# Performance work log

Measured on AMD Instinct MI355X. Metric: run time of the kernel, lower is better.

## Reference

```python
import jax, jax.numpy as jnp
import numpy as np
import math

N_HEAD = 12


def setup_inputs() -> dict:
    key = jax.random.key(0)
    ks = jax.random.split(key, 4)
    B, T, C = 8, 1024, 768
    s = 0.02
    return {
        "x": jax.random.normal(ks[0], (B, T, C), dtype=jnp.float32),
        "attn_mask": jnp.ones((B, T), dtype=jnp.int32),
        "W_attn": jax.random.normal(ks[1], (C, 3 * C), dtype=jnp.float32) * s,
        "b_attn": jnp.zeros((3 * C,), dtype=jnp.float32),
        "W_proj": jax.random.normal(ks[2], (C, C), dtype=jnp.float32) * s,
        "b_proj": jnp.zeros((C,), dtype=jnp.float32),
    }


def reference(x, attn_mask, W_attn, b_attn, W_proj, b_proj):
    B, T, C = x.shape
    hd = C // N_HEAD
    qkv = x @ W_attn + b_attn                      # [B, T, 3C]
    q, k, v = jnp.split(qkv, 3, axis=2)
    # [B, H, T, hd]
    q = q.reshape(B, T, N_HEAD, hd).transpose(0, 2, 1, 3)
    k = k.reshape(B, T, N_HEAD, hd).transpose(0, 2, 1, 3)
    v = v.reshape(B, T, N_HEAD, hd).transpose(0, 2, 1, 3)
    scores = jnp.einsum("bhqd,bhkd->bhqk", q, k) * (1.0 / math.sqrt(hd))
    mask = attn_mask[:, None, None, :]             # [B, 1, 1, T] broadcast over H, q
    scores = jnp.where(mask == 0, -jnp.inf, scores)
    attn = jax.nn.softmax(scores, axis=-1)
    out = jnp.einsum("bhqk,bhkd->bhqd", attn, v)   # [B, H, T, hd]
    out = out.transpose(0, 2, 1, 3).reshape(B, T, C)
    return out @ W_proj + b_proj
```

## Files before the change

kernel.cpp:

```cpp
#include <hip/hip_runtime.h>
#include <math.h>

constexpr int Bsz  = 8;
constexpr int Tseq = 1024;
constexpr int Cdim = 768;
constexpr int NH   = 12;
constexpr int HD   = 64;
constexpr int Mrows = Bsz * Tseq;
constexpr int C3    = 3 * Cdim;

using short8  = __attribute__((ext_vector_type(8))) short;
using s4v     = __attribute__((ext_vector_type(4))) short;
using floatx4 = __attribute__((ext_vector_type(4))) float;

__device__ __forceinline__ unsigned short f32_to_bf16_rn(float f) {
    unsigned int u = __float_as_uint(f);
    unsigned int r = u + 0x7FFFu + ((u >> 16) & 1u);
    return (unsigned short)(r >> 16);
}
__device__ __forceinline__ short8 lds_ld8(const unsigned short* p) {
    s4v a = *(const s4v*)p;
    s4v b = *(const s4v*)(p + 4);
    return __builtin_shufflevector(a, b, 0, 1, 2, 3, 4, 5, 6, 7);
}
__device__ __forceinline__ void lds_st8(unsigned short* p, short8 v) {
    *(s4v*)p       = __builtin_shufflevector(v, v, 0, 1, 2, 3);
    *(s4v*)(p + 4) = __builtin_shufflevector(v, v, 4, 5, 6, 7);
}

#define GLOAD_LDS16(g, l) __builtin_amdgcn_global_load_lds(                    \
    (const __attribute__((address_space(1))) void*)(g),                        \
    (__attribute__((address_space(3))) void*)(l), 16, 0, 0)

__global__ __launch_bounds__(256)
void to_bf16(const float* __restrict__ in, unsigned short* __restrict__ out, int n4)
{
    int t = blockIdx.x * blockDim.x + threadIdx.x;
    if (t >= n4) return;
    float4 v = ((const float4*)in)[t];
    ushort4 o;
    o.x = f32_to_bf16_rn(v.x);
    o.y = f32_to_bf16_rn(v.y);
    o.z = f32_to_bf16_rn(v.z);
    o.w = f32_to_bf16_rn(v.w);
    ((ushort4*)out)[t] = o;
}

__global__ __launch_bounds__(256)
void transpose_bf16(const float* __restrict__ in, unsigned short* __restrict__ out,
                    int K, int N)
{
    __shared__ float tile[32][33];
    const int k0 = blockIdx.y * 32, n0 = blockIdx.x * 32;
    const int tx = threadIdx.x & 31, ty = threadIdx.x >> 5;
    #pragma unroll
    for (int r = ty; r < 32; r += 8)
        tile[r][tx] = in[(size_t)(k0 + r) * N + n0 + tx];
    __syncthreads();
    #pragma unroll
    for (int r = ty; r < 32; r += 8)
        out[(size_t)(n0 + r) * K + k0 + tx] = f32_to_bf16_rn(tile[tx][r]);
}

__global__ __launch_bounds__(256)
void gemm_qkv(const unsigned short* __restrict__ A_g,
              const unsigned short* __restrict__ B_g,
              const float* __restrict__ bias,
              unsigned short* __restrict__ Cb,
              int M, int N, int K)
{
    __shared__ __align__(16) unsigned short Ah[128 * 32];
    __shared__ __align__(16) unsigned short Bh[128 * 32];

    const int tid  = threadIdx.x;
    const int wave = tid >> 6;
    const int lane = tid & 63;
    const int lm   = lane & 15;
    const int quad = lane >> 4;
    const int wy   = wave >> 1, wx = wave & 1;
    const int row0 = blockIdx.y * 128;
    const int col0 = blockIdx.x * 128;

    const int sr  = lane >> 2;
    const int skp = (lane & 3) * 8;

    floatx4 acc[4][4] = {};

    for (int k0 = 0; k0 < K; k0 += 32) {
        __syncthreads();
        #pragma unroll
        for (int s = 0; s < 2; ++s) {
            const int r = (wave * 2 + s) * 16 + sr;
            GLOAD_LDS16(A_g + (size_t)(row0 + r) * K + k0 + skp, &Ah[r * 32 + skp]);
            GLOAD_LDS16(B_g + (size_t)(col0 + r) * K + k0 + skp, &Bh[r * 32 + skp]);
        }
        __syncthreads();

        short8 af[4];
        #pragma unroll
        for (int i = 0; i < 4; ++i)
            af[i] = *(const short8*)&Ah[(wy * 64 + i * 16 + lm) * 32 + quad * 8];
        #pragma unroll
        for (int j = 0; j < 4; ++j) {
            short8 bf = *(const short8*)&Bh[(wx * 64 + j * 16 + lm) * 32 + quad * 8];
            #pragma unroll
            for (int i = 0; i < 4; ++i)
                acc[i][j] = __builtin_amdgcn_mfma_f32_16x16x32_bf16(af[i], bf, acc[i][j], 0, 0, 0);
        }
    }

    __syncthreads();
    unsigned short* wbuf = &Ah[wave * 1024];
    #pragma unroll
    for (int i = 0; i < 4; ++i) {
        #pragma unroll
        for (int j = 0; j < 4; ++j) {
            const float bv = bias[col0 + wx * 64 + j * 16 + lm];
            #pragma unroll
            for (int r = 0; r < 4; ++r)
                wbuf[(quad * 4 + r) * 64 + j * 16 + lm] = f32_to_bf16_rn(acc[i][j][r] + bv);
        }
        #pragma unroll
        for (int p = 0; p < 2; ++p) {
            const int lrow  = p * 8 + (lane >> 3);
            const int lcol8 = (lane & 7) * 8;
            short8 v = lds_ld8(&wbuf[lrow * 64 + lcol8]);
            lds_st8((unsigned short*)&v, v);
            *(short8*)(Cb + (size_t)(row0 + wy * 64 + i * 16 + lrow) * N +
                       col0 + wx * 64 + lcol8) = v;
        }
    }
}

__global__ __launch_bounds__(256)
void gemm_proj(const unsigned short* __restrict__ AO_g,
               const unsigned short* __restrict__ B_g,
               const float* __restrict__ bias,
               float* __restrict__ C,
               int M, int N, int K)
{
    __shared__ __align__(16) unsigned short Ah[128 * 32];
    __shared__ __align__(16) unsigned short Bh[128 * 32];

    const int tid  = threadIdx.x;
    const int wave = tid >> 6;
    const int lane = tid & 63;
    const int lm   = lane & 15;
    const int quad = lane >> 4;
    const int wy   = wave >> 1, wx = wave & 1;
    const int row0 = blockIdx.y * 128;
    const int col0 = blockIdx.x * 128;

    const int sr  = lane >> 2;
    const int skp = (lane & 3) * 8;

    floatx4 acc[4][4] = {};

    for (int k0 = 0; k0 < K; k0 += 32) {
        __syncthreads();
        const int kk   = k0 + skp;
        const int head = kk >> 6;
        const int off  = kk & 63;
        #pragma unroll
        for (int s = 0; s < 2; ++s) {
            const int r = (wave * 2 + s) * 16 + sr;
            GLOAD_LDS16(AO_g + (size_t)head * (Mrows * HD) + (size_t)(row0 + r) * HD + off,
                        &Ah[r * 32 + skp]);
            GLOAD_LDS16(B_g + (size_t)(col0 + r) * K + k0 + skp, &Bh[r * 32 + skp]);
        }
        __syncthreads();

        short8 af[4];
        #pragma unroll
        for (int i = 0; i < 4; ++i)
            af[i] = *(const short8*)&Ah[(wy * 64 + i * 16 + lm) * 32 + quad * 8];
        #pragma unroll
        for (int j = 0; j < 4; ++j) {
            short8 bf = *(const short8*)&Bh[(wx * 64 + j * 16 + lm) * 32 + quad * 8];
            #pragma unroll
            for (int i = 0; i < 4; ++i)
                acc[i][j] = __builtin_amdgcn_mfma_f32_16x16x32_bf16(af[i], bf, acc[i][j], 0, 0, 0);
        }
    }

    #pragma unroll
    for (int j = 0; j < 4; ++j) {
        const int col = col0 + wx * 64 + j * 16 + lm;
        const float bv = bias[col];
        #pragma unroll
        for (int i = 0; i < 4; ++i) {
            const int rowb = row0 + wy * 64 + i * 16 + quad * 4;
            #pragma unroll
            for (int r = 0; r < 4; ++r)
                C[(size_t)(rowb + r) * N + col] = acc[i][j][r] + bv;
        }
    }
}

__global__ __launch_bounds__(256, 2)
void attn_bf16(const unsigned short* __restrict__ qkv,
               const int* __restrict__ mask,
               unsigned short* __restrict__ outh)
{
    constexpr int LDW = 68;
    __shared__ __align__(16) unsigned short Kh[64 * LDW];
    __shared__ __align__(16) unsigned short Vh[64 * LDW];
    __shared__ __align__(16) unsigned short Ph[128 * LDW];
    __shared__ float maskadd[64];

    const int tid  = threadIdx.x;
    const int wave = tid >> 6;
    const int lane = tid & 63;
    const int lm   = lane & 15;
    const int quad = lane >> 4;
    const int idx  = blockIdx.x;
    const int bh   = idx % (Bsz * NH);
    const int qb   = idx / (Bsz * NH);
    const int b    = bh / NH;
    const int h    = bh % NH;
    const int q0   = qb * 128;
    const float scale = 0.125f;

    short8 qf[2][2];
    #pragma unroll
    for (int mt = 0; mt < 2; ++mt) {
        const size_t qrow = (size_t)(b * Tseq + q0 + wave * 32 + mt * 16 + lm) * C3 + h * HD;
        #pragma unroll
        for (int kf = 0; kf < 2; ++kf)
            qf[mt][kf] = *(const short8*)(qkv + qrow + kf * 32 + quad * 8);
    }

    const int sr0 = (tid & 31) * 2;
    const int sc  = (tid >> 5) * 8;

    short8 kh0, kh1, vh0, vh1;
    float  mreg = 0.f;

    {
        const size_t g0 = (size_t)(b * Tseq + sr0) * C3 + Cdim + h * HD + sc;
        kh0 = *(const short8*)(qkv + g0);
        kh1 = *(const short8*)(qkv + g0 + C3);
        vh0 = *(const short8*)(qkv + g0 + Cdim);
        vh1 = *(const short8*)(qkv + g0 + Cdim + C3);
        if (tid < 64) mreg = (mask[b * Tseq + tid] == 0) ? -1e30f : 0.0f;
        lds_st8(&Kh[sr0 * LDW + sc], kh0);
        lds_st8(&Kh[(sr0 + 1) * LDW + sc], kh1);
        #pragma unroll
        for (int i = 0; i < 8; ++i) {
            unsigned int pv = (unsigned int)(unsigned short)vh0[i] |
                              ((unsigned int)(unsigned short)vh1[i] << 16);
            *(unsigned int*)&Vh[(sc + i) * LDW + sr0] = pv;
        }
        if (tid < 64) maskadd[tid] = mreg;
    }
    __syncthreads();

    floatx4 O[2][4] = {};
    float lsum[2] = {0.f, 0.f};
    float madd[4][4];

    for (int kt = 0; kt < Tseq / 64; ++kt) {
        floatx4 S[2][4] = {};
        #pragma unroll
        for (int kf = 0; kf < 2; ++kf) {
            short8 kh[4];
            #pragma unroll
            for (int nt = 0; nt < 4; ++nt)
                kh[nt] = lds_ld8(&Kh[(nt * 16 + lm) * LDW + kf * 32 + quad * 8]);
            #pragma unroll
            for (int mt = 0; mt < 2; ++mt)
                #pragma unroll
                for (int nt = 0; nt < 4; ++nt)
                    S[mt][nt] = __builtin_amdgcn_mfma_f32_16x16x32_bf16(kh[nt], qf[mt][kf], S[mt][nt], 0, 0, 0);
        }
        #pragma unroll
        for (int nt = 0; nt < 4; ++nt)
            #pragma unroll
            for (int r = 0; r < 4; ++r)
                madd[nt][r] = maskadd[nt * 16 + quad * 4 + r];

        if (kt + 1 < Tseq / 64) {
            const size_t g0 = (size_t)(b * Tseq + (kt + 1) * 64 + sr0) * C3 + Cdim + h * HD + sc;
            kh0 = *(const short8*)(qkv + g0);
            kh1 = *(const short8*)(qkv + g0 + C3);
            vh0 = *(const short8*)(qkv + g0 + Cdim);
            vh1 = *(const short8*)(qkv + g0 + Cdim + C3);
            if (tid < 64) mreg = (mask[b * Tseq + (kt + 1) * 64 + tid] == 0) ? -1e30f : 0.0f;
        }

        #pragma unroll
        for (int mt = 0; mt < 2; ++mt) {
            const int prow = (wave * 32 + mt * 16 + lm) * LDW;
            #pragma unroll
            for (int nt = 0; nt < 4; ++nt) {
                ushort4 pk;
                unsigned short* pp = &pk.x;
                #pragma unroll
                for (int r = 0; r < 4; ++r) {
                    float p = __expf(S[mt][nt][r] * scale + madd[nt][r]);
                    lsum[mt] += p;
                    pp[r] = f32_to_bf16_rn(p);
                }
                *(ushort4*)&Ph[prow + nt * 16 + quad * 4] = pk;
            }
        }

        #pragma unroll
        for (int kf = 0; kf < 2; ++kf) {
            short8 pf[2];
            #pragma unroll
            for (int mt = 0; mt < 2; ++mt)
                pf[mt] = lds_ld8(&Ph[(wave * 32 + mt * 16 + lm) * LDW + kf * 32 + quad * 8]);
            #pragma unroll
            for (int dt = 0; dt < 4; ++dt) {
                short8 vh = lds_ld8(&Vh[(dt * 16 + lm) * LDW + kf * 32 + quad * 8]);
                #pragma unroll
                for (int mt = 0; mt < 2; ++mt)
                    O[mt][dt] = __builtin_amdgcn_mfma_f32_16x16x32_bf16(vh, pf[mt], O[mt][dt], 0, 0, 0);
            }
        }

        __syncthreads();
        if (kt + 1 < Tseq / 64) {
            lds_st8(&Kh[sr0 * LDW + sc], kh0);
            lds_st8(&Kh[(sr0 + 1) * LDW + sc], kh1);
            #pragma unroll
            for (int i = 0; i < 8; ++i) {
                unsigned int pv = (unsigned int)(unsigned short)vh0[i] |
                                  ((unsigned int)(unsigned short)vh1[i] << 16);
                *(unsigned int*)&Vh[(sc + i) * LDW + sr0] = pv;
            }
            if (tid < 64) maskadd[tid] = mreg;
        }
        __syncthreads();
    }

    #pragma unroll
    for (int mt = 0; mt < 2; ++mt) {
        lsum[mt] += __shfl_xor(lsum[mt], 16);
        lsum[mt] += __shfl_xor(lsum[mt], 32);
        const float inv_l = 1.0f / lsum[mt];
        const size_t row = (size_t)h * (Mrows * HD) +
                           (size_t)(b * Tseq + q0 + wave * 32 + mt * 16 + lm) * HD;
        #pragma unroll
        for (int dt = 0; dt < 4; ++dt) {
            ushort4 hv;
            unsigned short* hp = &hv.x;
            #pragma unroll
            for (int r = 0; r < 4; ++r)
                hp[r] = f32_to_bf16_rn(O[mt][dt][r] * inv_l);
            *(ushort4*)(outh + row + dt * 16 + quad * 4) = hv;
        }
    }
}

extern "C" void kernel_launch(void* const* d_in, const int* in_sizes, int n_in,
                              void* d_out, int out_size, void* d_ws, size_t ws_size,
                              hipStream_t stream)
{
    const float* x      = (const float*)d_in[0];
    const int*   mask   = (const int*)  d_in[1];
    const float* W_attn = (const float*)d_in[2];
    const float* b_attn = (const float*)d_in[3];
    const float* W_proj = (const float*)d_in[4];
    const float* b_proj = (const float*)d_in[5];
    float* out = (float*)d_out;

    unsigned short* xh    = (unsigned short*)d_ws;
    unsigned short* wat_h = xh    + (size_t)Mrows * Cdim;
    unsigned short* wpt_h = wat_h + (size_t)C3 * Cdim;
    unsigned short* qkvh  = wpt_h + (size_t)Cdim * Cdim;
    unsigned short* aoh   = xh;

    dim3 blk(256);

    to_bf16<<<dim3(Mrows * Cdim / 4 / 256), blk, 0, stream>>>(x, xh, Mrows * Cdim / 4);
    transpose_bf16<<<dim3(C3 / 32, Cdim / 32), blk, 0, stream>>>(W_attn, wat_h, Cdim, C3);
    transpose_bf16<<<dim3(Cdim / 32, Cdim / 32), blk, 0, stream>>>(W_proj, wpt_h, Cdim, Cdim);

    gemm_qkv<<<dim3(C3 / 128, Mrows / 128), blk, 0, stream>>>(
        xh, wat_h, b_attn, qkvh, Mrows, C3, Cdim);

    attn_bf16<<<dim3((Tseq / 128) * Bsz * NH), blk, 0, stream>>>(qkvh, mask, aoh);

    gemm_proj<<<dim3(Cdim / 128, Mrows / 128), blk, 0, stream>>>(
        aoh, wpt_h, b_proj, out, Mrows, Cdim, Cdim);
}
```

Baseline: 227.0 us.

## Double-buffer K/V tiles in attention and drop redundant LDS store in QKV epilogue

The attention kernel now keeps two LDS buffers each for K, V and the mask row. The next tile is written into the spare buffer while the current one is consumed, which removes one of the two __syncthreads per key tile. The global loads for the next tile are issued before the QK^T MFMAs so more work covers their latency. The QKV GEMM epilogue drops a stray self-store to LDS and adds explicit lgkmcnt waits. The extra buffers raise LDS use per block, which may reduce how many blocks fit on a CU.

```diff
diff --git a/kernel.cpp b/kernel.cpp
--- a/kernel.cpp
+++ b/kernel.cpp
@@ -120,15 +120,16 @@
             for (int r = 0; r < 4; ++r)
                 wbuf[(quad * 4 + r) * 64 + j * 16 + lm] = f32_to_bf16_rn(acc[i][j][r] + bv);
         }
+        asm volatile("s_waitcnt lgkmcnt(0)" ::: "memory");
         #pragma unroll
         for (int p = 0; p < 2; ++p) {
             const int lrow  = p * 8 + (lane >> 3);
             const int lcol8 = (lane & 7) * 8;
             short8 v = lds_ld8(&wbuf[lrow * 64 + lcol8]);
-            lds_st8((unsigned short*)&v, v);
             *(short8*)(Cb + (size_t)(row0 + wy * 64 + i * 16 + lrow) * N +
                        col0 + wx * 64 + lcol8) = v;
         }
+        asm volatile("s_waitcnt lgkmcnt(0)" ::: "memory");
     }
 }
 
@@ -203,10 +204,11 @@
                unsigned short* __restrict__ outh)
 {
     constexpr int LDW = 68;
-    __shared__ __align__(16) unsigned short Kh[64 * LDW];
-    __shared__ __align__(16) unsigned short Vh[64 * LDW];
+    constexpr int NT  = Tseq / 64;
+    __shared__ __align__(16) unsigned short Kh[2][64 * LDW];
+    __shared__ __align__(16) unsigned short Vh[2][64 * LDW];
     __shared__ __align__(16) unsigned short Ph[128 * LDW];
-    __shared__ float maskadd[64];
+    __shared__ float maskadd[2][64];
 
     const int tid  = threadIdx.x;
     const int wave = tid >> 6;
@@ -243,15 +245,15 @@
         vh0 = *(const short8*)(qkv + g0 + Cdim);
         vh1 = *(const short8*)(qkv + g0 + Cdim + C3);
         if (tid < 64) mreg = (mask[b * Tseq + tid] == 0) ? -1e30f : 0.0f;
-        lds_st8(&Kh[sr0 * LDW + sc], kh0);
-        lds_st8(&Kh[(sr0 + 1) * LDW + sc], kh1);
+        lds_st8(&Kh[0][sr0 * LDW + sc], kh0);
+        lds_st8(&Kh[0][(sr0 + 1) * LDW + sc], kh1);
         #pragma unroll
         for (int i = 0; i < 8; ++i) {
             unsigned int pv = (unsigned int)(unsigned short)vh0[i] |
                               ((unsigned int)(unsigned short)vh1[i] << 16);
-            *(unsigned int*)&Vh[(sc + i) * LDW + sr0] = pv;
-        }
-        if (tid < 64) maskadd[tid] = mreg;
+            *(unsigned int*)&Vh[0][(sc + i) * LDW + sr0] = pv;
+        }
+        if (tid < 64) maskadd[0][tid] = mreg;
     }
     __syncthreads();
 
@@ -259,27 +261,13 @@
     float lsum[2] = {0.f, 0.f};
     float madd[4][4];
 
-    for (int kt = 0; kt < Tseq / 64; ++kt) {
-        floatx4 S[2][4] = {};
-        #pragma unroll
-        for (int kf = 0; kf < 2; ++kf) {
-            short8 kh[4];
-            #pragma unroll
-            for (int nt = 0; nt < 4; ++nt)
-                kh[nt] = lds_ld8(&Kh[(nt * 16 + lm) * LDW + kf * 32 + quad * 8]);
-            #pragma unroll
-            for (int mt = 0; mt < 2; ++mt)
-                #pragma unroll
-                for (int nt = 0; nt < 4; ++nt)
-                    S[mt][nt] = __builtin_amdgcn_mfma_f32_16x16x32_bf16(kh[nt], qf[mt][kf], S[mt][nt], 0, 0, 0);
-        }
-        #pragma unroll
-        for (int nt = 0; nt < 4; ++nt)
-            #pragma unroll
-            for (int r = 0; r < 4; ++r)
-                madd[nt][r] = maskadd[nt * 16 + quad * 4 + r];
-
-        if (kt + 1 < Tseq / 64) {
+    for (int kt = 0; kt < NT; ++kt) {
+        const int cur = kt & 1;
+        const int nxt = cur ^ 1;
+        const unsigned short* Khc = Kh[cur];
+        const unsigned short* Vhc = Vh[cur];
+
+        if (kt + 1 < NT) {
             const size_t g0 = (size_t)(b * Tseq + (kt + 1) * 64 + sr0) * C3 + Cdim + h * HD + sc;
             kh0 = *(const short8*)(qkv + g0);
             kh1 = *(const short8*)(qkv + g0 + C3);
@@ -287,6 +275,25 @@
             vh1 = *(const short8*)(qkv + g0 + Cdim + C3);
             if (tid < 64) mreg = (mask[b * Tseq + (kt + 1) * 64 + tid] == 0) ? -1e30f : 0.0f;
         }
+
+        floatx4 S[2][4] = {};
+        #pragma unroll
+        for (int kf = 0; kf < 2; ++kf) {
+            short8 kh[4];
+            #pragma unroll
+            for (int nt = 0; nt < 4; ++nt)
+                kh[nt] = lds_ld8(&Khc[(nt * 16 + lm) * LDW + kf * 32 + quad * 8]);
+            #pragma unroll
+            for (int mt = 0; mt < 2; ++mt)
+                #pragma unroll
+                for (int nt = 0; nt < 4; ++nt)
+                    S[mt][nt] = __builtin_amdgcn_mfma_f32_16x16x32_bf16(kh[nt], qf[mt][kf], S[mt][nt], 0, 0, 0);
+        }
+        #pragma unroll
+        for (int nt = 0; nt < 4; ++nt)
+            #pragma unroll
+            for (int r = 0; r < 4; ++r)
+                madd[nt][r] = maskadd[cur][nt * 16 + quad * 4 + r];
 
         #pragma unroll
         for (int mt = 0; mt < 2; ++mt) {
@@ -313,24 +320,23 @@
                 pf[mt] = lds_ld8(&Ph[(wave * 32 + mt * 16 + lm) * LDW + kf * 32 + quad * 8]);
             #pragma unroll
             for (int dt = 0; dt < 4; ++dt) {
-                short8 vh = lds_ld8(&Vh[(dt * 16 + lm) * LDW + kf * 32 + quad * 8]);
+                short8 vh = lds_ld8(&Vhc[(dt * 16 + lm) * LDW + kf * 32 + quad * 8]);
                 #pragma unroll
                 for (int mt = 0; mt < 2; ++mt)
                     O[mt][dt] = __builtin_amdgcn_mfma_f32_16x16x32_bf16(vh, pf[mt], O[mt][dt], 0, 0, 0);
             }
         }
 
-        __syncthreads();
-        if (kt + 1 < Tseq / 64) {
-            lds_st8(&Kh[sr0 * LDW + sc], kh0);
-            lds_st8(&Kh[(sr0 + 1) * LDW + sc], kh1);
+        if (kt + 1 < NT) {
+            lds_st8(&Kh[nxt][sr0 * LDW + sc], kh0);
+            lds_st8(&Kh[nxt][(sr0 + 1) * LDW + sc], kh1);
             #pragma unroll
             for (int i = 0; i < 8; ++i) {
                 unsigned int pv = (unsigned int)(unsigned short)vh0[i] |
                                   ((unsigned int)(unsigned short)vh1[i] << 16);
-                *(unsigned int*)&Vh[(sc + i) * LDW + sr0] = pv;
+                *(unsigned int*)&Vh[nxt][(sc + i) * LDW + sr0] = pv;
             }
-            if (tid < 64) maskadd[tid] = mreg;
+            if (tid < 64) maskadd[nxt][tid] = mreg;
         }
         __syncthreads();
     }
```

Measured after the change: 214.2 us. 5.6% less time.
